# Performance work log

Hardware: AMD Instinct MI355X
Metric: run time of the kernel (lower is better)

Reference implementation:

```python
import jax, jax.numpy as jnp
import numpy as np

LN_EPS = 1e-5


def _linear(x, W, b):
    return x @ W + b


def _layernorm(x, g, b):
    mu = x.mean(-1, keepdims=True)
    var = ((x - mu) ** 2).mean(-1, keepdims=True)
    return (x - mu) * jax.lax.rsqrt(var + LN_EPS) * g + b


def setup_inputs() -> dict:
    key = jax.random.key(0)
    ks = jax.random.split(key, 12)
    B, N, D, S = 8, 40000, 256, 128
    hid = D // 4  # 64
    coordinates = jax.random.normal(ks[0], (B, N, 3), dtype=jnp.float32)
    features = jax.random.normal(ks[1], (B, N, D), dtype=jnp.float32)
    superpoint_labels = jax.random.randint(ks[2], (B, N), 0, S, dtype=jnp.int64)
    def w(k, fan_in, shape):
        return jax.random.normal(k, shape, dtype=jnp.float32) / np.sqrt(fan_in)
    return {
        "coordinates": coordinates,
        "features": features,
        "superpoint_labels": superpoint_labels,
        "num_superpoints": S,
        "W1": w(ks[3], 4, (4, hid)), "b1": jnp.zeros((hid,), jnp.float32),
        "W2": w(ks[4], hid, (hid, D)), "b2": jnp.zeros((D,), jnp.float32),
        "W3": w(ks[5], D, (D, D)), "b3": jnp.zeros((D,), jnp.float32),
        "ln_g": jnp.ones((D,), jnp.float32), "ln_b": jnp.zeros((D,), jnp.float32),
        "W4": w(ks[6], D, (D, D)), "b4": jnp.zeros((D,), jnp.float32),
    }


def _forward_one(coords, labels, S, W1, b1, W2, b2, W3, b3, ln_g, ln_b, W4, b4, D):
    # coords: [N,3], labels: [N] int in [0,S)
    N = coords.shape[0]
    ones = jnp.ones((N,), coords.dtype)
    counts = jax.ops.segment_sum(ones, labels, num_segments=S)          # [S]
    sums = jax.ops.segment_sum(coords, labels, num_segments=S)          # [S,3]
    centers = sums / jnp.maximum(counts, 1.0)[:, None]
    valid = counts >= 2.0                                                # torch: mask.sum() < 2 -> skip
    vmask = valid.astype(coords.dtype)
    nv = vmask.sum()
    # pairwise center distances (cdist), safe sqrt (zero grad at 0 like torch)
    d2 = ((centers[:, None, :] - centers[None, :, :]) ** 2).sum(-1)      # [S,S]
    dist = jnp.sqrt(jnp.where(d2 > 0, d2, 1.0)) * (d2 > 0)
    denom = jnp.maximum(nv, 1.0)
    mean_d = (dist * vmask[None, :]).sum(1) / denom                      # includes self (0), as in torch
    min_d = jnp.where(vmask[None, :] > 0, dist, jnp.inf).min(1)          # always 0 (self), as in torch
    z = centers[:, 2]
    frac = ((z[:, None] > z[None, :]).astype(coords.dtype) * vmask[None, :]).sum(1) / denom
    rel = jnp.stack([mean_d, min_d, z, frac], axis=1)                    # [S,4]
    h = _linear(jax.nn.gelu(_linear(rel, W1, b1), approximate=False), W2, b2)  # relation_mlp
    a = _linear(h, W3, b3)
    a = jax.nn.gelu(_layernorm(a, ln_g, ln_b), approximate=False)
    a = _linear(a, W4, b4)                                               # [S,D]
    enough = (nv >= 2.0).astype(coords.dtype)
    a = a * vmask[:, None] * enough                                      # invalid segments stay zero
    return a[labels]                                                     # scatter back per point [N,D]


def reference(coordinates, features, superpoint_labels, num_superpoints,
              W1, b1, W2, b2, W3, b3, ln_g, ln_b, W4, b4):
    B, N, D = features.shape
    S = int(num_superpoints)
    f = lambda c, l: _forward_one(c, l, S, W1, b1, W2, b2, W3, b3, ln_g, ln_b, W4, b4, D)
    return jax.vmap(f)(coordinates, superpoint_labels)
```

## Files before the change

kernel.cpp:

```cpp
#include <hip/hip_runtime.h>
#include <math.h>

#define S 128
#define D 256
#define HID 64
#define ROWS 4
#define LN_EPS 1e-5f

__device__ __forceinline__ float gelu_exact(float x) {
    return 0.5f * x * (1.0f + erff(x * 0.70710678118654752440f));
}

__global__ __launch_bounds__(256) void seg_sum_kernel(
    const float* __restrict__ coords,
    const int* __restrict__ labels,
    int* __restrict__ cnt,
    float* __restrict__ sums,
    int N, int chunks_per_batch)
{
    __shared__ int   scnt[S];
    __shared__ float sx[S], sy[S], sz[S];
    int t = threadIdx.x;
    if (t < S) { scnt[t] = 0; sx[t] = 0.f; sy[t] = 0.f; sz[t] = 0.f; }
    __syncthreads();

    int b     = blockIdx.x / chunks_per_batch;
    int chunk = blockIdx.x % chunks_per_batch;
    int per   = (N + chunks_per_batch - 1) / chunks_per_batch;
    int start = chunk * per;
    int end   = min(start + per, N);

    for (int i = start + t; i < end; i += blockDim.x) {
        int idx = b * N + i;
        int lbl = labels[idx];
        float x = coords[idx * 3 + 0];
        float y = coords[idx * 3 + 1];
        float z = coords[idx * 3 + 2];
        atomicAdd(&scnt[lbl], 1);
        atomicAdd(&sx[lbl], x);
        atomicAdd(&sy[lbl], y);
        atomicAdd(&sz[lbl], z);
    }
    __syncthreads();
    if (t < S && scnt[t] != 0) {
        atomicAdd(&cnt[b * S + t], scnt[t]);
        atomicAdd(&sums[(b * S + t) * 3 + 0], sx[t]);
        atomicAdd(&sums[(b * S + t) * 3 + 1], sy[t]);
        atomicAdd(&sums[(b * S + t) * 3 + 2], sz[t]);
    }
}

__global__ __launch_bounds__(S) void rel_kernel(
    const int* __restrict__ cnt,
    const float* __restrict__ sums,
    float* __restrict__ rel,
    float* __restrict__ scale)
{
    __shared__ float cx[S], cy[S], cz[S], vm[S];
    int b = blockIdx.x;
    int s = threadIdx.x;

    int c = cnt[b * S + s];
    float dc = fmaxf((float)c, 1.0f);
    float x = sums[(b * S + s) * 3 + 0] / dc;
    float y = sums[(b * S + s) * 3 + 1] / dc;
    float z = sums[(b * S + s) * 3 + 2] / dc;
    float v = (c >= 2) ? 1.0f : 0.0f;
    cx[s] = x; cy[s] = y; cz[s] = z; vm[s] = v;
    __syncthreads();

    float nv = 0.f, sum_d = 0.f, frac = 0.f, min_d = INFINITY;
    for (int j = 0; j < S; j++) {
        float dx = x - cx[j], dy = y - cy[j], dz = z - cz[j];
        float d2 = dx * dx + dy * dy + dz * dz;
        float dist = (d2 > 0.0f) ? sqrtf(d2) : 0.0f;
        float vj = vm[j];
        nv    += vj;
        sum_d += dist * vj;
        if (vj > 0.0f) min_d = fminf(min_d, dist);
        frac  += (z > cz[j]) ? vj : 0.0f;
    }
    float denom = fmaxf(nv, 1.0f);
    rel[(b * S + s) * 4 + 0] = sum_d / denom;
    rel[(b * S + s) * 4 + 1] = min_d;
    rel[(b * S + s) * 4 + 2] = z;
    rel[(b * S + s) * 4 + 3] = frac / denom;
    scale[b * S + s] = v * ((nv >= 2.0f) ? 1.0f : 0.0f);
}

__global__ __launch_bounds__(D) void mlp_kernel(
    const float* __restrict__ rel, const float* __restrict__ scale,
    const float* __restrict__ W1, const float* __restrict__ b1,
    const float* __restrict__ W2, const float* __restrict__ b2,
    const float* __restrict__ W3, const float* __restrict__ b3,
    const float* __restrict__ lng, const float* __restrict__ lnb,
    const float* __restrict__ W4, const float* __restrict__ b4,
    float* __restrict__ a_table)
{
    __shared__ float relS[ROWS][4];
    __shared__ float h1[ROWS][HID];
    __shared__ float h2[ROWS][D];
    __shared__ float red[4][ROWS][2];

    int t = threadIdx.x;
    int base = blockIdx.x * ROWS;

    if (t < ROWS * 4) relS[t >> 2][t & 3] = rel[base * 4 + t];
    __syncthreads();

    if (t < HID) {
        for (int r = 0; r < ROWS; r++) {
            float acc = b1[t];
            #pragma unroll
            for (int k = 0; k < 4; k++) acc += relS[r][k] * W1[k * HID + t];
            h1[r][t] = gelu_exact(acc);
        }
    }
    __syncthreads();

    {
        float acc[ROWS];
        #pragma unroll
        for (int r = 0; r < ROWS; r++) acc[r] = b2[t];
        for (int k = 0; k < HID; k++) {
            float w = W2[k * D + t];
            #pragma unroll
            for (int r = 0; r < ROWS; r++) acc[r] += h1[r][k] * w;
        }
        #pragma unroll
        for (int r = 0; r < ROWS; r++) h2[r][t] = acc[r];
    }
    __syncthreads();

    float a[ROWS];
    #pragma unroll
    for (int r = 0; r < ROWS; r++) a[r] = b3[t];
    for (int k = 0; k < D; k++) {
        float w = W3[k * D + t];
        #pragma unroll
        for (int r = 0; r < ROWS; r++) a[r] += h2[r][k] * w;
    }

    int wave = t >> 6, lane = t & 63;
    #pragma unroll
    for (int r = 0; r < ROWS; r++) {
        float s1 = a[r], s2 = a[r] * a[r];
        for (int off = 32; off > 0; off >>= 1) {
            s1 += __shfl_down(s1, off);
            s2 += __shfl_down(s2, off);
        }
        if (lane == 0) { red[wave][r][0] = s1; red[wave][r][1] = s2; }
    }
    __syncthreads();

    float xg[ROWS];
    float g = lng[t], bb = lnb[t];
    #pragma unroll
    for (int r = 0; r < ROWS; r++) {
        float s1 = red[0][r][0] + red[1][r][0] + red[2][r][0] + red[3][r][0];
        float s2 = red[0][r][1] + red[1][r][1] + red[2][r][1] + red[3][r][1];
        float mu  = s1 / (float)D;
        float var = s2 / (float)D - mu * mu;
        float ln = (a[r] - mu) * rsqrtf(var + LN_EPS) * g + bb;
        xg[r] = gelu_exact(ln);
    }
    __syncthreads();
    #pragma unroll
    for (int r = 0; r < ROWS; r++) h2[r][t] = xg[r];
    __syncthreads();

    float o[ROWS];
    #pragma unroll
    for (int r = 0; r < ROWS; r++) o[r] = b4[t];
    for (int k = 0; k < D; k++) {
        float w = W4[k * D + t];
        #pragma unroll
        for (int r = 0; r < ROWS; r++) o[r] += h2[r][k] * w;
    }
    #pragma unroll
    for (int r = 0; r < ROWS; r++) {
        a_table[(size_t)(base + r) * D + t] = o[r] * scale[base + r];
    }
}

__global__ __launch_bounds__(256) void gather_kernel(
    const int* __restrict__ labels,
    const float4* __restrict__ a_table,
    float4* __restrict__ out,
    int N, int total_rows)
{
    int row  = blockIdx.x * 4 + (threadIdx.x >> 6);
    int lane = threadIdx.x & 63;
    if (row >= total_rows) return;
    int b   = row / N;
    int lbl = labels[row];
    out[(size_t)row * 64 + lane] = a_table[(size_t)(b * S + lbl) * 64 + lane];
}

extern "C" void kernel_launch(void* const* d_in, const int* in_sizes, int n_in,
                              void* d_out, int out_size, void* d_ws, size_t ws_size,
                              hipStream_t stream) {
    const float* coords = (const float*)d_in[0];
    const int*   labels = (const int*)d_in[2];
    const float* W1 = (const float*)d_in[4];
    const float* b1 = (const float*)d_in[5];
    const float* W2 = (const float*)d_in[6];
    const float* b2 = (const float*)d_in[7];
    const float* W3 = (const float*)d_in[8];
    const float* b3 = (const float*)d_in[9];
    const float* lng = (const float*)d_in[10];
    const float* lnb = (const float*)d_in[11];
    const float* W4 = (const float*)d_in[12];
    const float* b4 = (const float*)d_in[13];

    const int B = 8;
    const int total_rows = in_sizes[2];
    const int N = total_rows / B;

    char* ws = (char*)d_ws;
    int*   cnt     = (int*)(ws + 0);
    float* sums    = (float*)(ws + 4096);
    float* rel     = (float*)(ws + 16384);
    float* scale   = (float*)(ws + 32768);
    float* a_table = (float*)(ws + 36864);

    hipMemsetAsync(ws, 0, 16384, stream);

    const int chunks = 32;
    seg_sum_kernel<<<B * chunks, 256, 0, stream>>>(coords, labels, cnt, sums, N, chunks);
    rel_kernel<<<B, S, 0, stream>>>(cnt, sums, rel, scale);
    mlp_kernel<<<(B * S) / ROWS, D, 0, stream>>>(rel, scale, W1, b1, W2, b2, W3, b3,
                                                 lng, lnb, W4, b4, a_table);
    gather_kernel<<<(total_rows + 3) / 4, 256, 0, stream>>>(
        labels, (const float4*)a_table, (float4*)d_out, N, total_rows);
}
```

Baseline: 534.7 us.

## Fuse segment reduction and relation features into MLP; grid-stride nontemporal gather

Segment sums are now written as per-chunk partials instead of global atomics, which removes the memset. The separate relation kernel is folded into the MLP kernel: each block reduces the partials and computes its four segments' relation features with wave-level reductions. The gather becomes a fixed-size grid-stride loop that uses nontemporal stores for the large output. This cuts two launches and the memset, but every MLP block now redundantly reduces all 32 partials for its batch.

Result: faster. 521.5 us (-2.5%).

```diff
diff --git a/kernel.cpp b/kernel.cpp
--- a/kernel.cpp
+++ b/kernel.cpp
@@ -5,18 +5,20 @@
 #define D 256
 #define HID 64
 #define ROWS 4
+#define CHUNKS 32
 #define LN_EPS 1e-5f
+
+typedef float v4 __attribute__((ext_vector_type(4)));
 
 __device__ __forceinline__ float gelu_exact(float x) {
     return 0.5f * x * (1.0f + erff(x * 0.70710678118654752440f));
 }
 
-__global__ __launch_bounds__(256) void seg_sum_kernel(
+__global__ __launch_bounds__(256) void seg_partial_kernel(
     const float* __restrict__ coords,
     const int* __restrict__ labels,
-    int* __restrict__ cnt,
-    float* __restrict__ sums,
-    int N, int chunks_per_batch)
+    float4* __restrict__ partial,
+    int N)
 {
     __shared__ int   scnt[S];
     __shared__ float sx[S], sy[S], sz[S];
@@ -24,9 +26,9 @@
     if (t < S) { scnt[t] = 0; sx[t] = 0.f; sy[t] = 0.f; sz[t] = 0.f; }
     __syncthreads();
 
-    int b     = blockIdx.x / chunks_per_batch;
-    int chunk = blockIdx.x % chunks_per_batch;
-    int per   = (N + chunks_per_batch - 1) / chunks_per_batch;
+    int b     = blockIdx.x / CHUNKS;
+    int chunk = blockIdx.x % CHUNKS;
+    int per   = (N + CHUNKS - 1) / CHUNKS;
     int start = chunk * per;
     int end   = min(start + per, N);
 
@@ -42,54 +44,15 @@
         atomicAdd(&sz[lbl], z);
     }
     __syncthreads();
-    if (t < S && scnt[t] != 0) {
-        atomicAdd(&cnt[b * S + t], scnt[t]);
-        atomicAdd(&sums[(b * S + t) * 3 + 0], sx[t]);
-        atomicAdd(&sums[(b * S + t) * 3 + 1], sy[t]);
-        atomicAdd(&sums[(b * S + t) * 3 + 2], sz[t]);
-    }
-}
-
-__global__ __launch_bounds__(S) void rel_kernel(
-    const int* __restrict__ cnt,
-    const float* __restrict__ sums,
-    float* __restrict__ rel,
-    float* __restrict__ scale)
-{
-    __shared__ float cx[S], cy[S], cz[S], vm[S];
-    int b = blockIdx.x;
-    int s = threadIdx.x;
-
-    int c = cnt[b * S + s];
-    float dc = fmaxf((float)c, 1.0f);
-    float x = sums[(b * S + s) * 3 + 0] / dc;
-    float y = sums[(b * S + s) * 3 + 1] / dc;
-    float z = sums[(b * S + s) * 3 + 2] / dc;
-    float v = (c >= 2) ? 1.0f : 0.0f;
-    cx[s] = x; cy[s] = y; cz[s] = z; vm[s] = v;
-    __syncthreads();
-
-    float nv = 0.f, sum_d = 0.f, frac = 0.f, min_d = INFINITY;
-    for (int j = 0; j < S; j++) {
-        float dx = x - cx[j], dy = y - cy[j], dz = z - cz[j];
-        float d2 = dx * dx + dy * dy + dz * dz;
-        float dist = (d2 > 0.0f) ? sqrtf(d2) : 0.0f;
-        float vj = vm[j];
-        nv    += vj;
-        sum_d += dist * vj;
-        if (vj > 0.0f) min_d = fminf(min_d, dist);
-        frac  += (z > cz[j]) ? vj : 0.0f;
-    }
-    float denom = fmaxf(nv, 1.0f);
-    rel[(b * S + s) * 4 + 0] = sum_d / denom;
-    rel[(b * S + s) * 4 + 1] = min_d;
-    rel[(b * S + s) * 4 + 2] = z;
-    rel[(b * S + s) * 4 + 3] = frac / denom;
-    scale[b * S + s] = v * ((nv >= 2.0f) ? 1.0f : 0.0f);
-}
-
-__global__ __launch_bounds__(D) void mlp_kernel(
-    const float* __restrict__ rel, const float* __restrict__ scale,
+    if (t < S) {
+        float4 p;
+        p.x = (float)scnt[t]; p.y = sx[t]; p.z = sy[t]; p.w = sz[t];
+        partial[(size_t)blockIdx.x * S + t] = p;
+    }
+}
+
+__global__ __launch_bounds__(256) void fused_mlp_kernel(
+    const float4* __restrict__ partial,
     const float* __restrict__ W1, const float* __restrict__ b1,
     const float* __restrict__ W2, const float* __restrict__ b2,
     const float* __restrict__ W3, const float* __restrict__ b3,
@@ -97,15 +60,62 @@
     const float* __restrict__ W4, const float* __restrict__ b4,
     float* __restrict__ a_table)
 {
+    __shared__ float cx[S], cy[S], cz[S], vm[S];
     __shared__ float relS[ROWS][4];
+    __shared__ float scaleS[ROWS];
     __shared__ float h1[ROWS][HID];
     __shared__ float h2[ROWS][D];
     __shared__ float red[4][ROWS][2];
 
     int t = threadIdx.x;
-    int base = blockIdx.x * ROWS;
-
-    if (t < ROWS * 4) relS[t >> 2][t & 3] = rel[base * 4 + t];
+    int b = blockIdx.x >> 5;
+    int base_seg = (blockIdx.x & 31) * ROWS;
+    int base_row = b * S + base_seg;
+
+    if (t < S) {
+        float4 acc = {0.f, 0.f, 0.f, 0.f};
+        for (int c = 0; c < CHUNKS; c++) {
+            float4 p = partial[(size_t)(b * CHUNKS + c) * S + t];
+            acc.x += p.x; acc.y += p.y; acc.z += p.z; acc.w += p.w;
+        }
+        float dc = fmaxf(acc.x, 1.0f);
+        cx[t] = acc.y / dc;
+        cy[t] = acc.z / dc;
+        cz[t] = acc.w / dc;
+        vm[t] = (acc.x >= 2.0f) ? 1.0f : 0.0f;
+    }
+    __syncthreads();
+
+    int wv = t >> 6, lane = t & 63;
+    {
+        int sg = base_seg + wv;
+        float x = cx[sg], y = cy[sg], z = cz[sg];
+        float nv = 0.f, sum_d = 0.f, frac = 0.f, min_d = INFINITY;
+        for (int j = lane; j < S; j += 64) {
+            float dx = x - cx[j], dy = y - cy[j], dz = z - cz[j];
+            float d2 = dx * dx + dy * dy + dz * dz;
+            float dist = (d2 > 0.0f) ? sqrtf(d2) : 0.0f;
+            float vj = vm[j];
+            nv    += vj;
+            sum_d += dist * vj;
+            if (vj > 0.0f) min_d = fminf(min_d, dist);
+            frac  += (z > cz[j]) ? vj : 0.0f;
+        }
+        for (int off = 32; off > 0; off >>= 1) {
+            nv    += __shfl_down(nv, off);
+            sum_d += __shfl_down(sum_d, off);
+            frac  += __shfl_down(frac, off);
+            min_d  = fminf(min_d, __shfl_down(min_d, off));
+        }
+        if (lane == 0) {
+            float denom = fmaxf(nv, 1.0f);
+            relS[wv][0] = sum_d / denom;
+            relS[wv][1] = min_d;
+            relS[wv][2] = z;
+            relS[wv][3] = frac / denom;
+            scaleS[wv]  = vm[sg] * ((nv >= 2.0f) ? 1.0f : 0.0f);
+        }
+    }
     __syncthreads();
 
     if (t < HID) {
@@ -141,7 +151,6 @@
         for (int r = 0; r < ROWS; r++) a[r] += h2[r][k] * w;
     }
 
-    int wave = t >> 6, lane = t & 63;
     #pragma unroll
     for (int r = 0; r < ROWS; r++) {
         float s1 = a[r], s2 = a[r] * a[r];
@@ -149,12 +158,12 @@
             s1 += __shfl_down(s1, off);
             s2 += __shfl_down(s2, off);
         }
-        if (lane == 0) { red[wave][r][0] = s1; red[wave][r][1] = s2; }
-    }
-    __syncthreads();
-
+        if (lane == 0) { red[wv][r][0] = s1; red[wv][r][1] = s2; }
+    }
+    __syncthreads();
+
+    float g = lng[t], bb = lnb[t];
     float xg[ROWS];
-    float g = lng[t], bb = lnb[t];
     #pragma unroll
     for (int r = 0; r < ROWS; r++) {
         float s1 = red[0][r][0] + red[1][r][0] + red[2][r][0] + red[3][r][0];
@@ -179,22 +188,28 @@
     }
     #pragma unroll
     for (int r = 0; r < ROWS; r++) {
-        a_table[(size_t)(base + r) * D + t] = o[r] * scale[base + r];
+        a_table[(size_t)(base_row + r) * D + t] = o[r] * scaleS[r];
     }
 }
 
 __global__ __launch_bounds__(256) void gather_kernel(
     const int* __restrict__ labels,
-    const float4* __restrict__ a_table,
-    float4* __restrict__ out,
-    int N, int total_rows)
+    const v4* __restrict__ a_table,
+    v4* __restrict__ out,
+    int N, int M)
 {
-    int row  = blockIdx.x * 4 + (threadIdx.x >> 6);
-    int lane = threadIdx.x & 63;
-    if (row >= total_rows) return;
-    int b   = row / N;
-    int lbl = labels[row];
-    out[(size_t)row * 64 + lane] = a_table[(size_t)(b * S + lbl) * 64 + lane];
+    int stride  = gridDim.x * blockDim.x;
+    int rowStep = stride >> 6;
+    int i    = blockIdx.x * blockDim.x + threadIdx.x;
+    int row  = i >> 6;
+    int lane = i & 63;
+    int b    = row / N;
+    for (; i < M; i += stride, row += rowStep) {
+        while (row >= (b + 1) * N) b++;
+        int lbl = labels[row];
+        v4 val = a_table[(size_t)((b << 7) + lbl) * 64 + lane];
+        __builtin_nontemporal_store(val, &out[i]);
+    }
 }
 
 extern "C" void kernel_launch(void* const* d_in, const int* in_sizes, int n_in,
@@ -218,19 +233,12 @@
     const int N = total_rows / B;
 
     char* ws = (char*)d_ws;
-    int*   cnt     = (int*)(ws + 0);
-    float* sums    = (float*)(ws + 4096);
-    float* rel     = (float*)(ws + 16384);
-    float* scale   = (float*)(ws + 32768);
-    float* a_table = (float*)(ws + 36864);
-
-    hipMemsetAsync(ws, 0, 16384, stream);
-
-    const int chunks = 32;
-    seg_sum_kernel<<<B * chunks, 256, 0, stream>>>(coords, labels, cnt, sums, N, chunks);
-    rel_kernel<<<B, S, 0, stream>>>(cnt, sums, rel, scale);
-    mlp_kernel<<<(B * S) / ROWS, D, 0, stream>>>(rel, scale, W1, b1, W2, b2, W3, b3,
-                                                 lng, lnb, W4, b4, a_table);
-    gather_kernel<<<(total_rows + 3) / 4, 256, 0, stream>>>(
-        labels, (const float4*)a_table, (float4*)d_out, N, total_rows);
-}
+    float4* partial = (float4*)(ws + 0);
+    float*  a_table = (float*)(ws + 524288);
+
+    seg_partial_kernel<<<B * CHUNKS, 256, 0, stream>>>(coords, labels, partial, N);
+    fused_mlp_kernel<<<(B * S) / ROWS, 256, 0, stream>>>(partial, W1, b1, W2, b2, W3, b3,
+                                                         lng, lnb, W4, b4, a_table);
+    int M = total_rows * (D / 4);
+    gather_kernel<<<2048, 256, 0, stream>>>(labels, (const v4*)a_table, (v4*)d_out, N, M);
+}
```
